# Optimization experiments

Hardware: AMD Instinct MI355X
Metric: run time of the kernel (lower is better)

Reference implementation:

```python
import jax, jax.numpy as jnp
import numpy as np

QLEN, MLEN = 1024, 1024
KLEN = QLEN + MLEN
BSZ = 2
D_MODEL = 1024
N_HEAD, D_HEAD = 16, 64


def setup_inputs() -> dict:
    key = jax.random.key(0)
    ks = jax.random.split(key, 8)
    s = 0.02
    return {
        "w": jax.random.normal(ks[0], (KLEN, BSZ, D_MODEL), jnp.float32),
        "r": jax.random.normal(ks[1], (KLEN, D_MODEL), jnp.float32),
        "r_w_bias": jax.random.normal(ks[2], (N_HEAD, D_HEAD), jnp.float32) * s,
        "r_r_bias": jax.random.normal(ks[3], (N_HEAD, D_HEAD), jnp.float32) * s,
        "Wq": jax.random.normal(ks[4], (D_MODEL, N_HEAD * D_HEAD), jnp.float32) * s,
        "Wkv": jax.random.normal(ks[5], (D_MODEL, 2 * N_HEAD * D_HEAD), jnp.float32) * s,
        "Wr": jax.random.normal(ks[6], (D_MODEL, N_HEAD * D_HEAD), jnp.float32) * s,
        "Wo": jax.random.normal(ks[7], (N_HEAD * D_HEAD, D_MODEL), jnp.float32) * s,
        "qlen": QLEN,
    }


def _rel_shift(x):
    # x: [qlen, klen, bsz, n_head]. Pad one zero column at the front of the
    # key axis, reinterpret flat layout as [klen+1, qlen, ...], drop row 0.
    q, k, b, n = x.shape
    x_pad = jnp.pad(x, ((0, 0), (1, 0), (0, 0), (0, 0)))
    return x_pad.reshape(k + 1, q, b, n)[1:].reshape(q, k, b, n)


def reference(w, r, r_w_bias, r_r_bias, Wq, Wkv, Wr, Wo, qlen):
    klen, bsz, _ = w.shape
    rlen = r.shape[0]
    scale = 1.0 / (D_HEAD ** 0.5)

    w_head_q = (w[-qlen:] @ Wq).reshape(qlen, bsz, N_HEAD, D_HEAD)
    kv = w @ Wkv
    w_head_k = kv[..., : N_HEAD * D_HEAD].reshape(klen, bsz, N_HEAD, D_HEAD)
    w_head_v = kv[..., N_HEAD * D_HEAD :].reshape(klen, bsz, N_HEAD, D_HEAD)
    r_head_k = (r @ Wr).reshape(rlen, N_HEAD, D_HEAD)

    AC = jnp.einsum("ibnd,jbnd->ijbn", w_head_q + r_w_bias, w_head_k)
    BD = jnp.einsum("ibnd,jnd->ijbn", w_head_q + r_r_bias, r_head_k)
    attn_score = (AC + _rel_shift(BD)) * scale

    attn_prob = jax.nn.softmax(attn_score, axis=1)
    attn_vec = jnp.einsum("ijbn,jbnd->ibnd", attn_prob, w_head_v)
    attn_vec = attn_vec.reshape(qlen, bsz, N_HEAD * D_HEAD)
    return attn_vec @ Wo
```

## Files before the change

kernel.cpp:

```cpp
#include <hip/hip_runtime.h>
#include <hip/hip_bf16.h>


#define QLENC 1024
#define KLENC 2048
#define BSZC 2
#define DMODELC 1024
#define NHC 16
#define DHC 64

typedef _Float16 half_t;
typedef __attribute__((ext_vector_type(8))) _Float16 f16x8;
typedef __attribute__((ext_vector_type(4))) float f32x4;

__device__ __forceinline__ void async_copy16(const half_t* g, half_t* l) {
    __builtin_amdgcn_global_load_lds(
        (const __attribute__((address_space(1))) void*)g,
        (__attribute__((address_space(3))) void*)l,
        16, 0, 0);
}

__global__ __launch_bounds__(256) void prep(
    const float* __restrict__ w, const float* __restrict__ r,
    const float* __restrict__ Wq, const float* __restrict__ Wkv,
    const float* __restrict__ Wr, const float* __restrict__ Wo,
    half_t* __restrict__ wh, half_t* __restrict__ rh,
    half_t* __restrict__ WqT, half_t* __restrict__ WkvT,
    half_t* __restrict__ WrT, half_t* __restrict__ WoT) {
    __shared__ __attribute__((aligned(16))) half_t T[64][72];
    int bx = blockIdx.x, t = threadIdx.x;
    if (bx < 3072) {
        const float* s; half_t* d; size_t base;
        if (bx < 2048) { s = w; d = wh; base = (size_t)bx * 2048; }
        else           { s = r; d = rh; base = (size_t)(bx - 2048) * 2048; }
        size_t i = base + (size_t)t * 8;
        const float4* sp = (const float4*)(s + i);
        float4 f0 = sp[0], f1 = sp[1];
        half_t h[8];
        h[0] = (half_t)f0.x; h[1] = (half_t)f0.y; h[2] = (half_t)f0.z; h[3] = (half_t)f0.w;
        h[4] = (half_t)f1.x; h[5] = (half_t)f1.y; h[6] = (half_t)f1.z; h[7] = (half_t)f1.w;
        *(uint4*)(d + i) = *(uint4*)&h[0];
        return;
    }
    int b2 = bx - 3072;
    const float* W; half_t* Wt; int N, tx, ty;
    if (b2 < 256)       { W = Wq;  Wt = WqT;  N = 1024; tx = b2 & 15;         ty = b2 >> 4; }
    else if (b2 < 768)  { int c = b2 - 256;  W = Wkv; Wt = WkvT; N = 2048; tx = c & 31; ty = c >> 5; }
    else if (b2 < 1024) { int c = b2 - 768;  W = Wr;  Wt = WrT;  N = 1024; tx = c & 15; ty = c >> 4; }
    else                { int c = b2 - 1024; W = Wo;  Wt = WoT;  N = 1024; tx = c & 15; ty = c >> 4; }
    const int K = 1024;
    int n0 = tx * 64, k0 = ty * 64;
    int r_ = t >> 2, c_ = (t & 3) << 4;
    const float4* s = (const float4*)&W[(size_t)(k0 + r_) * N + n0 + c_];
    float4 f0 = s[0], f1 = s[1], f2 = s[2], f3 = s[3];
    half_t h[16];
    h[0] = (half_t)f0.x; h[1] = (half_t)f0.y; h[2] = (half_t)f0.z; h[3] = (half_t)f0.w;
    h[4] = (half_t)f1.x; h[5] = (half_t)f1.y; h[6] = (half_t)f1.z; h[7] = (half_t)f1.w;
    h[8] = (half_t)f2.x; h[9] = (half_t)f2.y; h[10] = (half_t)f2.z; h[11] = (half_t)f2.w;
    h[12] = (half_t)f3.x; h[13] = (half_t)f3.y; h[14] = (half_t)f3.z; h[15] = (half_t)f3.w;
    *(uint4*)&T[r_][c_] = *(uint4*)&h[0];
    *(uint4*)&T[r_][c_ + 8] = *(uint4*)&h[8];
    __syncthreads();
    half_t vals[16];
#pragma unroll
    for (int u = 0; u < 16; u++) vals[u] = T[c_ + u][r_];
    *(uint4*)&Wt[(size_t)(n0 + r_) * K + k0 + c_] = *(uint4*)&vals[0];
    *(uint4*)&Wt[(size_t)(n0 + r_) * K + k0 + c_ + 8] = *(uint4*)&vals[8];
}

__global__ __launch_bounds__(256) void proj_fused(
    const half_t* __restrict__ wh, const half_t* __restrict__ rh,
    const half_t* __restrict__ WqT, const half_t* __restrict__ WkvT,
    const half_t* __restrict__ WrT,
    half_t* __restrict__ qw, half_t* __restrict__ qr,
    half_t* __restrict__ kh, half_t* __restrict__ vt,
    half_t* __restrict__ rk,
    const float* __restrict__ rwb, const float* __restrict__ rrb) {
    __shared__ __attribute__((aligned(16))) half_t As[128][64];
    __shared__ __attribute__((aligned(16))) half_t Bs[128][64];

    int bid = blockIdx.x;
    int mode, tx, ty;
    const half_t* A; const half_t* Bt;
    if (bid < 512)      { mode = 1; tx = bid & 15, ty = bid >> 4; A = wh; Bt = WkvT; }
    else if (bid < 640) { int c = bid - 512; mode = 0; tx = c & 7; ty = c >> 3;
                          A = wh + (size_t)QLENC * BSZC * DMODELC; Bt = WqT; }
    else                { int c = bid - 640; mode = 2; tx = c & 7; ty = c >> 3;
                          A = rh; Bt = WrT; }

    int t = threadIdx.x;
    int w = t >> 6, ln = t & 63, quad = ln >> 4, l15 = ln & 15;
    int m0 = ty * 128, n0 = tx * 128;
    int rbase = 64 * (w >> 1), cbase = 64 * (w & 1);
    int lrow = ln >> 3, lcol = (ln & 7) * 8;

    f32x4 acc[4][4];
#pragma unroll
    for (int i = 0; i < 4; i++)
#pragma unroll
        for (int j = 0; j < 4; j++) acc[i][j] = (f32x4){0.f, 0.f, 0.f, 0.f};

    for (int k0 = 0; k0 < 1024; k0 += 64) {
        __syncthreads();
#pragma unroll
        for (int j = 0; j < 4; j++) {
            int r8 = w * 32 + j * 8;
            async_copy16(&A[(size_t)(m0 + r8 + lrow) * 1024 + k0 + lcol], &As[r8][0]);
            async_copy16(&Bt[(size_t)(n0 + r8 + lrow) * 1024 + k0 + lcol], &Bs[r8][0]);
        }
        __syncthreads();
#pragma unroll
        for (int kk = 0; kk < 2; kk++) {
            f16x8 af[4], bfr[4];
#pragma unroll
            for (int rb = 0; rb < 4; rb++)
                af[rb] = *(const f16x8*)&As[rbase + rb * 16 + l15][kk * 32 + quad * 8];
#pragma unroll
            for (int cb = 0; cb < 4; cb++)
                bfr[cb] = *(const f16x8*)&Bs[cbase + cb * 16 + l15][kk * 32 + quad * 8];
#pragma unroll
            for (int rb = 0; rb < 4; rb++)
#pragma unroll
                for (int cb = 0; cb < 4; cb++)
                    acc[rb][cb] = __builtin_amdgcn_mfma_f32_16x16x32_f16(
                        af[rb], bfr[cb], acc[rb][cb], 0, 0, 0);
        }
    }

#pragma unroll
    for (int rb = 0; rb < 4; rb++)
#pragma unroll
        for (int cb = 0; cb < 4; cb++)
#pragma unroll
            for (int reg = 0; reg < 4; reg++) {
                int gr = m0 + rbase + 16 * rb + quad * 4 + reg;
                int gc = n0 + cbase + 16 * cb + l15;
                float v = acc[rb][cb][reg];
                if (mode == 1) {
                    int p_ = gr >> 1, b_ = gr & 1;
                    if (gc < NHC * DHC) {
                        int n_ = gc >> 6, d_ = gc & 63;
                        kh[(((size_t)(b_ * NHC + n_)) * KLENC + p_) * DHC + d_] = (half_t)v;
                    } else {
                        int c2 = gc - NHC * DHC, n_ = c2 >> 6, d_ = c2 & 63;
                        vt[(((size_t)(b_ * NHC + n_)) * DHC + d_) * KLENC + p_] = (half_t)v;
                    }
                } else if (mode == 0) {
                    int p_ = gr >> 1, b_ = gr & 1, n_ = gc >> 6, d_ = gc & 63;
                    size_t idx = (((size_t)(b_ * NHC + n_)) * QLENC + p_) * DHC + d_;
                    qw[idx] = (half_t)(v + rwb[gc]);
                    qr[idx] = (half_t)(v + rrb[gc]);
                } else {
                    int n_ = gc >> 6, d_ = gc & 63;
                    rk[(((size_t)n_) * KLENC + gr) * DHC + d_] = (half_t)v;
                }
            }
}

__global__ __launch_bounds__(256) void gemm_out(
    const half_t* __restrict__ A, const half_t* __restrict__ Bt,
    float* __restrict__ o) {
    __shared__ __attribute__((aligned(16))) half_t As[128][64];
    __shared__ __attribute__((aligned(16))) half_t Bs[128][64];

    int t = threadIdx.x;
    int w = t >> 6, ln = t & 63, quad = ln >> 4, l15 = ln & 15;
    int m0 = blockIdx.y * 128, n0 = blockIdx.x * 128;
    int rbase = 64 * (w >> 1), cbase = 64 * (w & 1);
    int lrow = ln >> 3, lcol = (ln & 7) * 8;

    f32x4 acc[4][4];
#pragma unroll
    for (int i = 0; i < 4; i++)
#pragma unroll
        for (int j = 0; j < 4; j++) acc[i][j] = (f32x4){0.f, 0.f, 0.f, 0.f};

    for (int k0 = 0; k0 < 1024; k0 += 64) {
        __syncthreads();
#pragma unroll
        for (int j = 0; j < 4; j++) {
            int r8 = w * 32 + j * 8;
            async_copy16(&A[(size_t)(m0 + r8 + lrow) * 1024 + k0 + lcol], &As[r8][0]);
            async_copy16(&Bt[(size_t)(n0 + r8 + lrow) * 1024 + k0 + lcol], &Bs[r8][0]);
        }
        __syncthreads();
#pragma unroll
        for (int kk = 0; kk < 2; kk++) {
            f16x8 af[4], bfr[4];
#pragma unroll
            for (int rb = 0; rb < 4; rb++)
                af[rb] = *(const f16x8*)&As[rbase + rb * 16 + l15][kk * 32 + quad * 8];
#pragma unroll
            for (int cb = 0; cb < 4; cb++)
                bfr[cb] = *(const f16x8*)&Bs[cbase + cb * 16 + l15][kk * 32 + quad * 8];
#pragma unroll
            for (int rb = 0; rb < 4; rb++)
#pragma unroll
                for (int cb = 0; cb < 4; cb++)
                    acc[rb][cb] = __builtin_amdgcn_mfma_f32_16x16x32_f16(
                        af[rb], bfr[cb], acc[rb][cb], 0, 0, 0);
        }
    }

#pragma unroll
    for (int rb = 0; rb < 4; rb++)
#pragma unroll
        for (int cb = 0; cb < 4; cb++)
#pragma unroll
            for (int reg = 0; reg < 4; reg++) {
                int gr = m0 + rbase + 16 * rb + quad * 4 + reg;
                int gc = n0 + cbase + 16 * cb + l15;
                o[(size_t)gr * 1024 + gc] = acc[rb][cb][reg];
            }
}

__global__ __launch_bounds__(256, 3) void attn_fused(
    const half_t* __restrict__ qw, const half_t* __restrict__ qr,
    const half_t* __restrict__ kh, const half_t* __restrict__ vt,
    const half_t* __restrict__ rk, half_t* __restrict__ av) {
    __shared__ __attribute__((aligned(16))) half_t Ks[64][72];
    __shared__ __attribute__((aligned(16))) half_t Vs[64][72];
    __shared__ __attribute__((aligned(16))) half_t RKs[128][72];
    __shared__ __attribute__((aligned(16))) half_t TP[4][16][88];

    int n = blockIdx.x, i0 = blockIdx.y * 64, b = blockIdx.z;
    int t = threadIdx.x, w = t >> 6, ln = t & 63, quad = ln >> 4, l15 = ln & 15;
    int lr = t >> 2, lc = (t & 3) << 4;
    int q4 = quad * 4;
    int wq = w * 16 + q4;
    size_t bn = (size_t)(b * NHC + n);
    const half_t* rkn = rk + (size_t)n * KLENC * DHC;
    half_t (*TPw)[88] = TP[w];

    f16x8 aqw[2], aq1[2], aq2[2];
    {
        int row1 = i0 + w * 16 + l15;
        int row2 = row1 + 1; if (row2 > QLENC - 1) row2 = QLENC - 1;
#pragma unroll
        for (int kk = 0; kk < 2; kk++) {
            aqw[kk] = *(const f16x8*)&qw[((bn * QLENC) + row1) * DHC + kk * 32 + quad * 8];
            aq1[kk] = *(const f16x8*)&qr[((bn * QLENC) + row1) * DHC + kk * 32 + quad * 8];
            aq2[kk] = *(const f16x8*)&qr[((bn * QLENC) + row2) * DHC + kk * 32 + quad * 8];
        }
    }

    int rrl = t >> 1, rh = (t & 1) * 32;

    uint4 pk0, pk1, pv0, pv1, pr0, pr1, pr2, pr3;
    {
        int D = 0 - i0;
        int mb = (D <= 1024) ? (960 + D) : (D - 1089);
        int rrow = mb + rrl; rrow = rrow < 0 ? 0 : (rrow > KLENC - 1 ? KLENC - 1 : rrow);
        const uint4* ks = (const uint4*)&kh[((bn * KLENC) + 0 + lr) * DHC + lc];
        const uint4* vs = (const uint4*)&vt[((bn * DHC) + lr) * KLENC + 0 + lc];
        pk0 = ks[0]; pk1 = ks[1]; pv0 = vs[0]; pv1 = vs[1];
        const uint4* rs = (const uint4*)&rkn[(size_t)rrow * DHC + rh];
        pr0 = rs[0]; pr1 = rs[1]; pr2 = rs[2]; pr3 = rs[3];
    }

    f32x4 O[4];
#pragma unroll
    for (int i = 0; i < 4; i++) O[i] = (f32x4){0.f, 0.f, 0.f, 0.f};
    float lsum[4] = {0.f, 0.f, 0.f, 0.f};
    const float scale = 0.125f;

    for (int jt = 0; jt < KLENC / 64; jt++) {
        int j0 = jt * 64;
        int D = j0 - i0;
        bool need1 = (D <= 1024), need2 = (D >= 1024);

        __syncthreads();
        *(uint4*)&Ks[lr][lc] = pk0; *(uint4*)&Ks[lr][lc + 8] = pk1;
        *(uint4*)&Vs[lr][lc] = pv0; *(uint4*)&Vs[lr][lc + 8] = pv1;
        *(uint4*)&RKs[rrl][rh] = pr0;      *(uint4*)&RKs[rrl][rh + 8] = pr1;
        *(uint4*)&RKs[rrl][rh + 16] = pr2; *(uint4*)&RKs[rrl][rh + 24] = pr3;
        __syncthreads();

        if (jt + 1 < KLENC / 64) {
            int j0n = j0 + 64, Dn = j0n - i0;
            int mbn = (Dn <= 1024) ? (960 + Dn) : (Dn - 1089);
            int rrown = mbn + rrl; rrown = rrown < 0 ? 0 : (rrown > KLENC - 1 ? KLENC - 1 : rrown);
            const uint4* ks = (const uint4*)&kh[((bn * KLENC) + j0n + lr) * DHC + lc];
            const uint4* vs = (const uint4*)&vt[((bn * DHC) + lr) * KLENC + j0n + lc];
            pk0 = ks[0]; pk1 = ks[1]; pv0 = vs[0]; pv1 = vs[1];
            const uint4* rs = (const uint4*)&rkn[(size_t)rrown * DHC + rh];
            pr0 = rs[0]; pr1 = rs[1]; pr2 = rs[2]; pr3 = rs[3];
        }

        f32x4 sa[4];
#pragma unroll
        for (int cb = 0; cb < 4; cb++) sa[cb] = (f32x4){0.f, 0.f, 0.f, 0.f};
#pragma unroll
        for (int kk = 0; kk < 2; kk++) {
#pragma unroll
            for (int cb = 0; cb < 4; cb++) {
                f16x8 bk = *(const f16x8*)&Ks[cb * 16 + l15][kk * 32 + quad * 8];
                sa[cb] = __builtin_amdgcn_mfma_f32_16x16x32_f16(aqw[kk], bk, sa[cb], 0, 0, 0);
            }
        }

        float bdv[4][4];
#pragma unroll
        for (int cb = 0; cb < 4; cb++)
#pragma unroll
            for (int reg = 0; reg < 4; reg++) bdv[cb][reg] = 0.f;

        if (need1) {
            f32x4 tacc[5];
#pragma unroll
            for (int c = 0; c < 5; c++) tacc[c] = (f32x4){0.f, 0.f, 0.f, 0.f};
#pragma unroll
            for (int kk = 0; kk < 2; kk++) {
#pragma unroll
                for (int c = 0; c < 5; c++) {
                    f16x8 bk = *(const f16x8*)&RKs[(3 - w + c) * 16 + l15][kk * 32 + quad * 8];
                    tacc[c] = __builtin_amdgcn_mfma_f32_16x16x32_f16(aq1[kk], bk, tacc[c], 0, 0, 0);
                }
            }
#pragma unroll
            for (int c = 0; c < 5; c++)
#pragma unroll
                for (int reg = 0; reg < 4; reg++)
                    TPw[q4 + reg][c * 16 + l15] = (half_t)tacc[c][reg];
#pragma unroll
            for (int reg = 0; reg < 4; reg++) {
                int icl = q4 + reg, ic = w * 16 + icl;
#pragma unroll
                for (int cb = 0; cb < 4; cb++) {
                    int jc = cb * 16 + l15;
                    int delta = D + jc - ic;
                    if (delta <= 1024) bdv[cb][reg] = (float)TPw[icl][15 + jc - icl];
                }
            }
        }
        if (need2) {
            if (need1) {
                int mb2 = D - 1089;
                int rrow2 = mb2 + rrl; rrow2 = rrow2 < 0 ? 0 : (rrow2 > KLENC - 1 ? KLENC - 1 : rrow2);
                const uint4* rs2 = (const uint4*)&rkn[(size_t)rrow2 * DHC + rh];
                uint4 t0 = rs2[0], t1 = rs2[1], t2 = rs2[2], t3 = rs2[3];
                __syncthreads();
                *(uint4*)&RKs[rrl][rh] = t0;      *(uint4*)&RKs[rrl][rh + 8] = t1;
                *(uint4*)&RKs[rrl][rh + 16] = t2; *(uint4*)&RKs[rrl][rh + 24] = t3;
                __syncthreads();
            }
            f32x4 tacc[5];
#pragma unroll
            for (int c = 0; c < 5; c++) tacc[c] = (f32x4){0.f, 0.f, 0.f, 0.f};
#pragma unroll
            for (int kk = 0; kk < 2; kk++) {
#pragma unroll
                for (int c = 0; c < 5; c++) {
                    f16x8 bk = *(const f16x8*)&RKs[(3 - w + c) * 16 + l15][kk * 32 + quad * 8];
                    tacc[c] = __builtin_amdgcn_mfma_f32_16x16x32_f16(aq2[kk], bk, tacc[c], 0, 0, 0);
                }
            }
#pragma unroll
            for (int c = 0; c < 5; c++)
#pragma unroll
                for (int reg = 0; reg < 4; reg++)
                    TPw[q4 + reg][c * 16 + l15] = (half_t)tacc[c][reg];
#pragma unroll
            for (int reg = 0; reg < 4; reg++) {
                int icl = q4 + reg, ic = w * 16 + icl;
#pragma unroll
                for (int cb = 0; cb < 4; cb++) {
                    int jc = cb * 16 + l15;
                    int delta = D + jc - ic;
                    if (delta >= 1026) bdv[cb][reg] = (float)TPw[icl][15 + jc - icl];
                }
            }
        }

        float p[4][4];
#pragma unroll
        for (int reg = 0; reg < 4; reg++) {
            float ps = 0.f;
#pragma unroll
            for (int cb = 0; cb < 4; cb++) {
                float e = __expf((sa[cb][reg] + bdv[cb][reg]) * scale);
                e = fminf(e, 60000.f);
                p[cb][reg] = e; ps += e;
            }
            lsum[reg] += ps;
        }

#pragma unroll
        for (int cb = 0; cb < 4; cb++)
#pragma unroll
            for (int reg = 0; reg < 4; reg++)
                TPw[q4 + reg][cb * 16 + l15] = (half_t)p[cb][reg];
#pragma unroll
        for (int kk = 0; kk < 2; kk++) {
            f16x8 pa = *(const f16x8*)&TPw[l15][kk * 32 + quad * 8];
#pragma unroll
            for (int db = 0; db < 4; db++) {
                f16x8 vb = *(const f16x8*)&Vs[db * 16 + l15][kk * 32 + quad * 8];
                O[db] = __builtin_amdgcn_mfma_f32_16x16x32_f16(pa, vb, O[db], 0, 0, 0);
            }
        }
    }

    float inv[4];
#pragma unroll
    for (int reg = 0; reg < 4; reg++) {
        float tot = lsum[reg];
#pragma unroll
        for (int off = 1; off < 16; off <<= 1) tot += __shfl_xor(tot, off, 64);
        inv[reg] = 1.0f / tot;
    }
#pragma unroll
    for (int db = 0; db < 4; db++)
#pragma unroll
        for (int reg = 0; reg < 4; reg++) {
            int i = i0 + wq + reg;
            int col = n * 64 + db * 16 + l15;
            av[((size_t)i * BSZC + b) * DMODELC + col] = (half_t)(O[db][reg] * inv[reg]);
        }
}

extern "C" void kernel_launch(void* const* d_in, const int* in_sizes, int n_in,
                              void* d_out, int out_size, void* d_ws, size_t ws_size,
                              hipStream_t stream) {
    const float* w   = (const float*)d_in[0];
    const float* r   = (const float*)d_in[1];
    const float* rwb = (const float*)d_in[2];
    const float* rrb = (const float*)d_in[3];
    const float* Wq  = (const float*)d_in[4];
    const float* Wkv = (const float*)d_in[5];
    const float* Wr  = (const float*)d_in[6];
    const float* Wo  = (const float*)d_in[7];
    float* out = (float*)d_out;

    half_t* ws = (half_t*)d_ws;
    half_t* qw   = ws; ws += (size_t)BSZC * NHC * QLENC * DHC;
    half_t* qr   = ws; ws += (size_t)BSZC * NHC * QLENC * DHC;
    half_t* kh   = ws; ws += (size_t)BSZC * NHC * KLENC * DHC;
    half_t* vt   = ws; ws += (size_t)BSZC * NHC * KLENC * DHC;
    half_t* rk   = ws; ws += (size_t)NHC * KLENC * DHC;
    half_t* av   = ws; ws += (size_t)QLENC * BSZC * DMODELC;
    half_t* WqT  = ws; ws += (size_t)DMODELC * DMODELC;
    half_t* WkvT = ws; ws += (size_t)2 * DMODELC * DMODELC;
    half_t* WrT  = ws; ws += (size_t)DMODELC * DMODELC;
    half_t* WoT  = ws; ws += (size_t)DMODELC * DMODELC;
    half_t* wh   = ws; ws += (size_t)KLENC * BSZC * DMODELC;
    half_t* rh   = ws; ws += (size_t)KLENC * DMODELC;

    dim3 blk(256);
    prep<<<dim3(4352), blk, 0, stream>>>(w, r, Wq, Wkv, Wr, Wo,
                                         wh, rh, WqT, WkvT, WrT, WoT);
    proj_fused<<<dim3(768), blk, 0, stream>>>(
        wh, rh, WqT, WkvT, WrT, qw, qr, kh, vt, rk, rwb, rrb);
    attn_fused<<<dim3(NHC, QLENC / 64, BSZC), blk, 0, stream>>>(
        qw, qr, kh, vt, rk, av);
    gemm_out<<<dim3(8, 16), blk, 0, stream>>>(av, WoT, out);

    (void)in_sizes; (void)n_in; (void)out_size; (void)ws_size;
}
```

Measured before the change: 279.0 us.

## Split attention key range across two blocks and load relative keys directly

The attention kernel now splits the key dimension into two halves, one per block, which doubles the grid from 512 to 1024 blocks. A new combine kernel sums the partial outputs and row sums and normalizes them. The relative-key tile no longer goes through shared memory. Each lane loads its MFMA B fragments straight from global memory, which drops the RKs buffer and the extra barrier pair. The partial buffers reuse the weight-transpose workspace, so WoT was moved ahead of it. In exchange this adds fp32 partial traffic, an extra launch, and uncoalesced, unpipelined global loads of the relative keys inside the loop.

```diff
diff --git a/kernel.cpp b/kernel.cpp
--- a/kernel.cpp
+++ b/kernel.cpp
@@ -217,13 +217,15 @@
 __global__ __launch_bounds__(256, 3) void attn_fused(
     const half_t* __restrict__ qw, const half_t* __restrict__ qr,
     const half_t* __restrict__ kh, const half_t* __restrict__ vt,
-    const half_t* __restrict__ rk, half_t* __restrict__ av) {
+    const half_t* __restrict__ rk, float* __restrict__ po,
+    float* __restrict__ pl) {
     __shared__ __attribute__((aligned(16))) half_t Ks[64][72];
     __shared__ __attribute__((aligned(16))) half_t Vs[64][72];
-    __shared__ __attribute__((aligned(16))) half_t RKs[128][72];
     __shared__ __attribute__((aligned(16))) half_t TP[4][16][88];
 
-    int n = blockIdx.x, i0 = blockIdx.y * 64, b = blockIdx.z;
+    int n = blockIdx.x, i0 = blockIdx.y * 64;
+    int z = blockIdx.z, b = z >> 1, s = z & 1;
+    int jt0 = s * 16;
     int t = threadIdx.x, w = t >> 6, ln = t & 63, quad = ln >> 4, l15 = ln & 15;
     int lr = t >> 2, lc = (t & 3) << 4;
     int q4 = quad * 4;
@@ -244,18 +246,12 @@
         }
     }
 
-    int rrl = t >> 1, rh = (t & 1) * 32;
-
-    uint4 pk0, pk1, pv0, pv1, pr0, pr1, pr2, pr3;
+    uint4 pk0, pk1, pv0, pv1;
     {
-        int D = 0 - i0;
-        int mb = (D <= 1024) ? (960 + D) : (D - 1089);
-        int rrow = mb + rrl; rrow = rrow < 0 ? 0 : (rrow > KLENC - 1 ? KLENC - 1 : rrow);
-        const uint4* ks = (const uint4*)&kh[((bn * KLENC) + 0 + lr) * DHC + lc];
-        const uint4* vs = (const uint4*)&vt[((bn * DHC) + lr) * KLENC + 0 + lc];
+        int j0 = jt0 * 64;
+        const uint4* ks = (const uint4*)&kh[((bn * KLENC) + j0 + lr) * DHC + lc];
+        const uint4* vs = (const uint4*)&vt[((bn * DHC) + lr) * KLENC + j0 + lc];
         pk0 = ks[0]; pk1 = ks[1]; pv0 = vs[0]; pv1 = vs[1];
-        const uint4* rs = (const uint4*)&rkn[(size_t)rrow * DHC + rh];
-        pr0 = rs[0]; pr1 = rs[1]; pr2 = rs[2]; pr3 = rs[3];
     }
 
     f32x4 O[4];
@@ -264,7 +260,7 @@
     float lsum[4] = {0.f, 0.f, 0.f, 0.f};
     const float scale = 0.125f;
 
-    for (int jt = 0; jt < KLENC / 64; jt++) {
+    for (int jt = jt0; jt < jt0 + 16; jt++) {
         int j0 = jt * 64;
         int D = j0 - i0;
         bool need1 = (D <= 1024), need2 = (D >= 1024);
@@ -272,19 +268,24 @@
         __syncthreads();
         *(uint4*)&Ks[lr][lc] = pk0; *(uint4*)&Ks[lr][lc + 8] = pk1;
         *(uint4*)&Vs[lr][lc] = pv0; *(uint4*)&Vs[lr][lc + 8] = pv1;
-        *(uint4*)&RKs[rrl][rh] = pr0;      *(uint4*)&RKs[rrl][rh + 8] = pr1;
-        *(uint4*)&RKs[rrl][rh + 16] = pr2; *(uint4*)&RKs[rrl][rh + 24] = pr3;
-        __syncthreads();
-
-        if (jt + 1 < KLENC / 64) {
-            int j0n = j0 + 64, Dn = j0n - i0;
-            int mbn = (Dn <= 1024) ? (960 + Dn) : (Dn - 1089);
-            int rrown = mbn + rrl; rrown = rrown < 0 ? 0 : (rrown > KLENC - 1 ? KLENC - 1 : rrown);
+        __syncthreads();
+
+        int mbA = need1 ? (960 + D) : (D - 1089);
+        f16x8 rkf[10];
+#pragma unroll
+        for (int c = 0; c < 5; c++) {
+            int rg = mbA + (3 - w + c) * 16 + l15;
+            rg = rg < 0 ? 0 : (rg > KLENC - 1 ? KLENC - 1 : rg);
+            const half_t* rp = &rkn[(size_t)rg * DHC + quad * 8];
+            rkf[c * 2]     = *(const f16x8*)rp;
+            rkf[c * 2 + 1] = *(const f16x8*)(rp + 32);
+        }
+
+        if (jt + 1 < jt0 + 16) {
+            int j0n = j0 + 64;
             const uint4* ks = (const uint4*)&kh[((bn * KLENC) + j0n + lr) * DHC + lc];
             const uint4* vs = (const uint4*)&vt[((bn * DHC) + lr) * KLENC + j0n + lc];
             pk0 = ks[0]; pk1 = ks[1]; pv0 = vs[0]; pv1 = vs[1];
-            const uint4* rs = (const uint4*)&rkn[(size_t)rrown * DHC + rh];
-            pr0 = rs[0]; pr1 = rs[1]; pr2 = rs[2]; pr3 = rs[3];
         }
 
         f32x4 sa[4];
@@ -305,17 +306,16 @@
 #pragma unroll
             for (int reg = 0; reg < 4; reg++) bdv[cb][reg] = 0.f;
 
-        if (need1) {
+        {
+            f16x8 aqA0 = need1 ? aq1[0] : aq2[0];
+            f16x8 aqA1 = need1 ? aq1[1] : aq2[1];
             f32x4 tacc[5];
 #pragma unroll
             for (int c = 0; c < 5; c++) tacc[c] = (f32x4){0.f, 0.f, 0.f, 0.f};
 #pragma unroll
-            for (int kk = 0; kk < 2; kk++) {
-#pragma unroll
-                for (int c = 0; c < 5; c++) {
-                    f16x8 bk = *(const f16x8*)&RKs[(3 - w + c) * 16 + l15][kk * 32 + quad * 8];
-                    tacc[c] = __builtin_amdgcn_mfma_f32_16x16x32_f16(aq1[kk], bk, tacc[c], 0, 0, 0);
-                }
+            for (int c = 0; c < 5; c++) {
+                tacc[c] = __builtin_amdgcn_mfma_f32_16x16x32_f16(aqA0, rkf[c * 2], tacc[c], 0, 0, 0);
+                tacc[c] = __builtin_amdgcn_mfma_f32_16x16x32_f16(aqA1, rkf[c * 2 + 1], tacc[c], 0, 0, 0);
             }
 #pragma unroll
             for (int c = 0; c < 5; c++)
@@ -329,31 +329,28 @@
                 for (int cb = 0; cb < 4; cb++) {
                     int jc = cb * 16 + l15;
                     int delta = D + jc - ic;
-                    if (delta <= 1024) bdv[cb][reg] = (float)TPw[icl][15 + jc - icl];
+                    bool take = need1 ? (delta <= 1024) : (delta >= 1026);
+                    if (take) bdv[cb][reg] = (float)TPw[icl][15 + jc - icl];
                 }
             }
         }
-        if (need2) {
-            if (need1) {
-                int mb2 = D - 1089;
-                int rrow2 = mb2 + rrl; rrow2 = rrow2 < 0 ? 0 : (rrow2 > KLENC - 1 ? KLENC - 1 : rrow2);
-                const uint4* rs2 = (const uint4*)&rkn[(size_t)rrow2 * DHC + rh];
-                uint4 t0 = rs2[0], t1 = rs2[1], t2 = rs2[2], t3 = rs2[3];
-                __syncthreads();
-                *(uint4*)&RKs[rrl][rh] = t0;      *(uint4*)&RKs[rrl][rh + 8] = t1;
-                *(uint4*)&RKs[rrl][rh + 16] = t2; *(uint4*)&RKs[rrl][rh + 24] = t3;
-                __syncthreads();
+        if (need1 && need2) {
+            int mbB = D - 1089;
+#pragma unroll
+            for (int c = 0; c < 5; c++) {
+                int rg = mbB + (3 - w + c) * 16 + l15;
+                rg = rg < 0 ? 0 : (rg > KLENC - 1 ? KLENC - 1 : rg);
+                const half_t* rp = &rkn[(size_t)rg * DHC + quad * 8];
+                rkf[c * 2]     = *(const f16x8*)rp;
+                rkf[c * 2 + 1] = *(const f16x8*)(rp + 32);
             }
             f32x4 tacc[5];
 #pragma unroll
             for (int c = 0; c < 5; c++) tacc[c] = (f32x4){0.f, 0.f, 0.f, 0.f};
 #pragma unroll
-            for (int kk = 0; kk < 2; kk++) {
-#pragma unroll
-                for (int c = 0; c < 5; c++) {
-                    f16x8 bk = *(const f16x8*)&RKs[(3 - w + c) * 16 + l15][kk * 32 + quad * 8];
-                    tacc[c] = __builtin_amdgcn_mfma_f32_16x16x32_f16(aq2[kk], bk, tacc[c], 0, 0, 0);
-                }
+            for (int c = 0; c < 5; c++) {
+                tacc[c] = __builtin_amdgcn_mfma_f32_16x16x32_f16(aq2[0], rkf[c * 2], tacc[c], 0, 0, 0);
+                tacc[c] = __builtin_amdgcn_mfma_f32_16x16x32_f16(aq2[1], rkf[c * 2 + 1], tacc[c], 0, 0, 0);
             }
 #pragma unroll
             for (int c = 0; c < 5; c++)
@@ -401,22 +398,43 @@
         }
     }
 
-    float inv[4];
+    size_t pobase = ((size_t)s * 32 + bn) * QLENC;
+#pragma unroll
+    for (int db = 0; db < 4; db++)
+#pragma unroll
+        for (int reg = 0; reg < 4; reg++)
+            po[(pobase + i0 + wq + reg) * 64 + db * 16 + l15] = O[db][reg];
 #pragma unroll
     for (int reg = 0; reg < 4; reg++) {
         float tot = lsum[reg];
 #pragma unroll
         for (int off = 1; off < 16; off <<= 1) tot += __shfl_xor(tot, off, 64);
-        inv[reg] = 1.0f / tot;
-    }
-#pragma unroll
-    for (int db = 0; db < 4; db++)
-#pragma unroll
-        for (int reg = 0; reg < 4; reg++) {
-            int i = i0 + wq + reg;
-            int col = n * 64 + db * 16 + l15;
-            av[((size_t)i * BSZC + b) * DMODELC + col] = (half_t)(O[db][reg] * inv[reg]);
-        }
+        if (l15 == 0) pl[pobase + i0 + wq + reg] = tot;
+    }
+}
+
+__global__ __launch_bounds__(256) void combine(
+    const float* __restrict__ po, const float* __restrict__ pl,
+    half_t* __restrict__ av) {
+    int gid = blockIdx.x * 256 + threadIdx.x;
+    int d0 = (gid & 7) * 8;
+    int i = (gid >> 3) & 1023;
+    int bn = gid >> 13;
+    size_t rowoff = (size_t)bn * QLENC + i;
+    size_t base = rowoff * 64 + d0;
+    const size_t S = (size_t)32 * QLENC * 64;
+    float4 a0 = *(const float4*)&po[base];
+    float4 a1 = *(const float4*)&po[base + 4];
+    float4 b0 = *(const float4*)&po[S + base];
+    float4 b1 = *(const float4*)&po[S + base + 4];
+    float invl = 1.0f / (pl[rowoff] + pl[(size_t)32 * QLENC + rowoff]);
+    half_t h[8];
+    h[0] = (half_t)((a0.x + b0.x) * invl); h[1] = (half_t)((a0.y + b0.y) * invl);
+    h[2] = (half_t)((a0.z + b0.z) * invl); h[3] = (half_t)((a0.w + b0.w) * invl);
+    h[4] = (half_t)((a1.x + b1.x) * invl); h[5] = (half_t)((a1.y + b1.y) * invl);
+    h[6] = (half_t)((a1.z + b1.z) * invl); h[7] = (half_t)((a1.w + b1.w) * invl);
+    int b = bn >> 4, n = bn & 15;
+    *(uint4*)&av[((size_t)i * BSZC + b) * DMODELC + n * 64 + d0] = *(uint4*)&h[0];
 }
 
 extern "C" void kernel_launch(void* const* d_in, const int* in_sizes, int n_in,
@@ -439,20 +457,24 @@
     half_t* vt   = ws; ws += (size_t)BSZC * NHC * KLENC * DHC;
     half_t* rk   = ws; ws += (size_t)NHC * KLENC * DHC;
     half_t* av   = ws; ws += (size_t)QLENC * BSZC * DMODELC;
+    half_t* WoT  = ws; ws += (size_t)DMODELC * DMODELC;
     half_t* WqT  = ws; ws += (size_t)DMODELC * DMODELC;
     half_t* WkvT = ws; ws += (size_t)2 * DMODELC * DMODELC;
     half_t* WrT  = ws; ws += (size_t)DMODELC * DMODELC;
-    half_t* WoT  = ws; ws += (size_t)DMODELC * DMODELC;
     half_t* wh   = ws; ws += (size_t)KLENC * BSZC * DMODELC;
     half_t* rh   = ws; ws += (size_t)KLENC * DMODELC;
+
+    float* po = (float*)WqT;
+    float* pl = po + (size_t)2 * 32 * QLENC * 64;
 
     dim3 blk(256);
     prep<<<dim3(4352), blk, 0, stream>>>(w, r, Wq, Wkv, Wr, Wo,
                                          wh, rh, WqT, WkvT, WrT, WoT);
     proj_fused<<<dim3(768), blk, 0, stream>>>(
         wh, rh, WqT, WkvT, WrT, qw, qr, kh, vt, rk, rwb, rrb);
-    attn_fused<<<dim3(NHC, QLENC / 64, BSZC), blk, 0, stream>>>(
-        qw, qr, kh, vt, rk, av);
+    attn_fused<<<dim3(NHC, QLENC / 64, BSZC * 2), blk, 0, stream>>>(
+        qw, qr, kh, vt, rk, po, pl);
+    combine<<<dim3(1024), blk, 0, stream>>>(po, pl, av);
     gemm_out<<<dim3(8, 16), blk, 0, stream>>>(av, WoT, out);
 
     (void)in_sizes; (void)n_in; (void)out_size; (void)ws_size;
```

Measured after the change: 307.9 us. 1.1x slower.
